# Performance work log

Measured on AMD Instinct MI355X. Metric: run time of the kernel, lower is better.

The kernel has to match this reference:

```python
import jax, jax.numpy as jnp
import numpy as np

ALPHA, BETA = 0.5, 0.25
DELTA_AGG, DELTA_DIS = 0.5, 3.0
OHEM_RATIO = 3
MAX_INST = 8  # instance ids in [0, MAX_INST); 0 = background
NEG_INF = -1e10


def _safe_norm(sq):
    # sqrt with zero-safe gradient; returns 0 where sq == 0
    return jnp.sqrt(jnp.where(sq > 0, sq, 1.0)) * (sq > 0)


def _agg_dis_single(sim, gt_text, gt_kernel):
    # sim: [4, N] float, gt_text/gt_kernel: [N] int32 instance ids
    lab = jnp.arange(1, MAX_INST)                                  # [K]
    kmask = (gt_kernel[None, :] == lab[:, None]).astype(sim.dtype)  # [K, N]
    tmask = gt_text[None, :] == lab[:, None]                        # [K, N] bool
    kcount = kmask.sum(1)
    tcount = tmask.sum(1).astype(sim.dtype)
    valid = (kcount > 0) & (tcount > 0)                             # [K]
    # per-instance kernel centroid G_kernel: masked segment mean of sim vectors
    G = (kmask @ sim.T) / jnp.maximum(kcount, 1.0)[:, None]         # [K, 4]
    # loss_agg: distance of each text pixel's sim vector to its kernel centroid
    diff = sim.T[None, :, :] - G[:, None, :]                        # [K, N, 4]
    d = _safe_norm(jnp.sum(diff * diff, -1))                        # [K, N]
    D = jnp.square(jnp.maximum(d - DELTA_AGG, 0.0))
    per_inst = jnp.sum(jnp.log1p(D) * tmask, 1) / jnp.maximum(tcount, 1.0)
    n_valid = jnp.sum(valid)
    loss_agg = jnp.sum(jnp.where(valid, per_inst, 0.0)) / jnp.maximum(n_valid, 1).astype(sim.dtype)
    # loss_dis: pairwise discrimination between valid kernel centroids
    gd = G[:, None, :] - G[None, :, :]                              # [K, K, 4]
    gnorm = _safe_norm(jnp.sum(gd * gd, -1))
    Dij = jnp.square(jnp.maximum(DELTA_DIS - gnorm, 0.0))
    K = MAX_INST - 1
    idx = jnp.arange(K)
    pair = valid[:, None] & valid[None, :] & (idx[:, None] < idx[None, :])
    s = jnp.sum(jnp.where(pair, jnp.log1p(Dij), 0.0))
    denom = (n_valid * (n_valid - 1)).astype(sim.dtype)  # matches torch: n*(n-1), not #pairs
    loss_dis = jnp.where(n_valid > 1, s / jnp.maximum(denom, 1.0), 0.0)
    return loss_agg, loss_dis


def _ohem_single(score, gt, tm):
    # score/tm: [N] float, gt: [N] int — all flattened
    pos = gt > 0.5
    pos_num = jnp.sum(pos) - jnp.sum(pos & (tm <= 0.5))
    neg = ~pos
    neg_total = jnp.sum(neg)
    neg_num = jnp.minimum(pos_num * OHEM_RATIO, neg_total)
    neg_scores = jnp.where(neg, score, NEG_INF)
    sorted_desc = -jnp.sort(-neg_scores)
    threshold = sorted_desc[jnp.maximum(neg_num - 1, 0)]
    sel = (((score >= threshold) | pos) & (tm > 0.5)).astype(tm.dtype)
    fallback = (pos_num == 0) | (neg_num == 0)
    return jnp.where(fallback, tm, sel)


def _dice(inp, tgt, mask):
    # inp: [B, N] logits, tgt: [B, N] (binarized at 0.5), mask: [B, N]
    p = jax.nn.sigmoid(inp) * mask
    t = (tgt > 0.5).astype(p.dtype) * mask
    a = jnp.sum(p * t, 1)
    b = jnp.sum(p * p, 1) + 1e-3
    c = jnp.sum(t * t, 1) + 1e-3
    return 1.0 - 2.0 * a / (b + c)


def _pan_loss(outputs, labels, training_masks):
    B = outputs.shape[0]
    texts = outputs[:, 0].reshape(B, -1)
    kernels = outputs[:, 1].reshape(B, -1)
    sim = outputs[:, 2:].reshape(B, 4, -1)
    gt_texts = labels[:, 0].reshape(B, -1)
    gt_kernels = labels[:, 1].reshape(B, -1)
    tm = training_masks.reshape(B, -1)

    loss_aggs, loss_diss = jax.vmap(_agg_dis_single)(sim, gt_texts, gt_kernels)

    # OHEM mask is computed on detached scores in the original (numpy round-trip)
    sel_text = jax.vmap(_ohem_single)(jax.lax.stop_gradient(texts), gt_texts, tm)
    loss_texts = _dice(texts, gt_texts, sel_text)

    sel_kernel = jax.lax.stop_gradient(
        ((jax.nn.sigmoid(texts) > 0.5) & (tm > 0.5)).astype(texts.dtype))
    loss_kernels = _dice(kernels, gt_kernels, sel_kernel)

    loss_text = loss_texts.mean()
    loss_kernel = loss_kernels.mean()
    loss_agg = loss_aggs.mean()
    loss_dis = loss_diss.mean()
    loss_all = loss_text + ALPHA * loss_kernel + BETA * (loss_agg + loss_dis)
    return loss_all, loss_text, loss_kernel, loss_agg, loss_dis


def setup_inputs() -> dict:
    key = jax.random.key(0)
    k1, k2, k3 = jax.random.split(key, 3)
    B, H, W = 8, 640, 640
    outputs = jax.random.normal(k1, (B, 6, H, W), dtype=jnp.float32)
    labels = jax.random.randint(k2, (B, 2, H, W), 0, MAX_INST).astype(jnp.int32)
    training_masks = jax.random.uniform(k3, (B, H, W), dtype=jnp.float32)
    return {"outputs": outputs, "labels": labels, "training_masks": training_masks}


def reference(outputs, labels, training_masks):
    return _pan_loss(outputs, labels, training_masks)
```

## Files before the change

kernel.cpp:

```cpp
#include <hip/hip_runtime.h>

#define NPIX 409600
#define NB 8

constexpr int OFF_H0   = 0;
constexpr int OFF_H1   = 2048;
constexpr int OFF_H2   = 4096;
constexpr int OFF_KC   = 5120;
constexpr int OFF_TC   = 5128;
constexpr int OFF_KS   = 5136;
constexpr int OFF_AGG  = 5168;
constexpr int OFF_CPOS = 5176;
constexpr int OFF_CPOSM= 5177;
constexpr int OFF_KN   = 5178;
constexpr int OFF_KNF  = 5179;
constexpr int OFF_FALL = 5180;
constexpr int OFF_NV   = 5181;
constexpr int OFF_VM   = 5182;
constexpr int OFF_LDIS = 5183;
constexpr int OFF_BTN  = 5184;
constexpr int OFF_PFX0 = 5185;
constexpr int OFF_K1   = 5186;
constexpr int OFF_PFX22= 5187;
constexpr int OFF_K2   = 5188;
constexpr int OFF_DICE = 5190;
constexpr int PER_BATCH= 5248;
constexpr int KEYS_BASE= NB * PER_BATCH;
constexpr int HDR_WORDS= NB * PER_BATCH;

__device__ __forceinline__ unsigned mapf(float s) {
  unsigned b = __float_as_uint(s);
  return (b & 0x80000000u) ? ~b : (b | 0x80000000u);
}
__device__ __forceinline__ float unmapf(unsigned u) {
  return __uint_as_float((u & 0x80000000u) ? (u & 0x7FFFFFFFu) : ~u);
}
__device__ __forceinline__ float sigf(float x) {
  return __fdividef(1.f, 1.f + __expf(-x));
}
__device__ __forceinline__ float wredf(float v) {
#pragma unroll
  for (int m = 32; m >= 1; m >>= 1) v += __shfl_xor(v, m, 64);
  return v;
}
__device__ __forceinline__ unsigned wredu(unsigned v) {
#pragma unroll
  for (int m = 32; m >= 1; m >>= 1) v += (unsigned)__shfl_xor((int)v, m, 64);
  return v;
}

__global__ __launch_bounds__(256) void kZ(unsigned* __restrict__ ws) {
  int i = blockIdx.x * 256 + threadIdx.x;
  if (i < HDR_WORDS) ws[i] = 0u;
}

__global__ __launch_bounds__(256) void kXS(const float* __restrict__ out_,
                                           const int* __restrict__ lab_,
                                           const float* __restrict__ tm_,
                                           unsigned* __restrict__ ws) {
  const int b = blockIdx.y;
  unsigned* wsb = ws + (size_t)b * PER_BATCH;
  float* wsbf = (float*)wsb;
  __shared__ __align__(16) unsigned shm[4412];
  const int tid = threadIdx.x, lane = tid & 63, w = tid >> 6;

  if (blockIdx.x < 200) {
    const int bx = blockIdx.x;
    unsigned* sh_h   = shm;
    unsigned* shScan = shm + 2048;
    unsigned* shTC   = shm + 2304;
    float*    shRed  = (float*)(shm + 2336);
    unsigned* shC    = shm + 2372;
    unsigned* shBase = shm + 2380;
    for (int i = tid; i < 2048; i += 256) sh_h[i] = 0u;
    __syncthreads();

    const float4* tx = (const float4*)(out_ + (size_t)b * 6 * NPIX);
    const float4* kr = (const float4*)(out_ + (size_t)b * 6 * NPIX + (size_t)NPIX);
    const int4* gt = (const int4*)(lab_ + (size_t)b * 2 * NPIX);
    const int4* gk = (const int4*)(lab_ + (size_t)b * 2 * NPIX + NPIX);
    const float4* tmv = (const float4*)(tm_ + (size_t)b * NPIX);

    unsigned cpos = 0, cposm = 0, vmask = 0, fmask = 0;
    unsigned tcq[7];
#pragma unroll
    for (int k = 0; k < 7; ++k) tcq[k] = 0u;
    unsigned kreg[8];
    float at = 0.f, btp = 0.f, ct = 0.f, atf = 0.f, btf = 0.f, ctf = 0.f;
    float ak = 0.f, bk = 0.f, ck = 0.f;

#pragma unroll
    for (int it = 0; it < 2; ++it) {
      const int i = it * 51200 + bx * 256 + tid;
      float4 t4 = tx[i]; float4 q4 = kr[i]; int4 g4 = gt[i]; int4 k4 = gk[i]; float4 m4 = tmv[i];
#pragma unroll
      for (int j = 0; j < 4; ++j) {
        float tv = ((const float*)&t4)[j];
        float kv = ((const float*)&q4)[j];
        int gtv = ((const int*)&g4)[j];
        int gkv = ((const int*)&k4)[j];
        float mv = ((const float*)&m4)[j];
        bool pos = gtv > 0;
        bool mh = mv > 0.5f;
        cpos += pos;
        cposm += (pos && !mh);
        unsigned key = mapf(tv);
        kreg[it * 4 + j] = key;
        float sig = sigf(tv);
        if (!pos) {
          vmask |= 1u << (it * 4 + j);
          if (mh) fmask |= 1u << (it * 4 + j);
          atomicAdd(&sh_h[key >> 21], 1u);
        } else if (mh) {
          at += sig; btp += sig * sig; ct += 1.f;
        }
#pragma unroll
        for (int k = 0; k < 7; ++k)
          tcq[k] += (unsigned)__popcll(__ballot(gtv == k + 1));
        float sm = sig * mv;
        btf += sm * sm;
        if (pos) { atf += sm * mv; ctf += mv * mv; }
        if ((tv > 0.f) && mh) {
          float sk = sigf(kv);
          bk += sk * sk;
          if (gkv > 0) { ak += sk; ck += 1.f; }
        }
      }
    }

    unsigned r = wredu(cpos), r2 = wredu(cposm);
    if (lane == 0) { shC[w * 2] = r; shC[w * 2 + 1] = r2; }
    if (lane == 0) {
#pragma unroll
      for (int k = 0; k < 7; ++k) shTC[w * 7 + k] = tcq[k];
    }
    float v9[9] = {at, btp, ct, atf, btf, ctf, ak, bk, ck};
#pragma unroll
    for (int q = 0; q < 9; ++q) {
      float f = wredf(v9[q]);
      if (lane == 0) shRed[w * 9 + q] = f;
    }

    unsigned cnt = (unsigned)__popc(vmask), cntF = (unsigned)__popc(fmask);
    shScan[tid] = cnt | (cntF << 16);
    __syncthreads();
#pragma unroll
    for (int off = 1; off < 256; off <<= 1) {
      unsigned vv = (tid >= off) ? shScan[tid - off] : 0u;
      __syncthreads();
      shScan[tid] += vv;
      __syncthreads();
    }
    if (tid == 0) {
      unsigned tot = shScan[255];
      shBase[0] = atomicAdd(&wsb[OFF_KN], tot & 0xFFFFu);
      shBase[1] = atomicAdd(&wsb[OFF_KNF], tot >> 16);
    }
    for (int i = tid; i < 2048; i += 256) {
      unsigned h = sh_h[i]; if (h) atomicAdd(&wsb[OFF_H0 + i], h);
    }
    if (tid < 7) {
      unsigned s = shTC[tid] + shTC[7 + tid] + shTC[14 + tid] + shTC[21 + tid];
      if (s) atomicAdd(&wsb[OFF_TC + 1 + tid], s);
    } else if (tid >= 16 && tid < 25) {
      int q = tid - 16;
      float s = shRed[q] + shRed[9 + q] + shRed[18 + q] + shRed[27 + q];
      atomicAdd(&wsbf[OFF_DICE + q], s);
    } else if (tid == 30) {
      atomicAdd(&wsb[OFF_CPOS], shC[0] + shC[2] + shC[4] + shC[6]);
    } else if (tid == 31) {
      atomicAdd(&wsb[OFF_CPOSM], shC[1] + shC[3] + shC[5] + shC[7]);
    }
    __syncthreads();
    unsigned gA = shBase[0] + (shScan[tid] & 0xFFFFu) - cnt;
    unsigned gF = shBase[1] + (shScan[tid] >> 16) - cntF;
    unsigned* keys = ws + KEYS_BASE + (size_t)b * NPIX;
#pragma unroll
    for (int s = 0; s < 8; ++s)
      if (vmask & (1u << s)) { keys[gA] = kreg[s]; ++gA; }
#pragma unroll
    for (int s = 0; s < 8; ++s)
      if (fmask & (1u << s)) { keys[NPIX - 1 - gF] = kreg[s]; ++gF; }
  } else {
    const bool lo = blockIdx.x < 328;
    const int bx = lo ? (blockIdx.x - 200) : (blockIdx.x - 328);
    float* L = (float*)shm;
    float* L2 = (float*)(shm + 4112);
    unsigned* sh_kcw = shm + 4384;
    for (int i = tid; i < 4112; i += 256) L[i] = 0.f;
    __syncthreads();

    const float4* sa = (const float4*)(out_ + (size_t)b * 6 * NPIX + (size_t)(lo ? 2 : 4) * NPIX);
    const float4* sb = (const float4*)(out_ + (size_t)b * 6 * NPIX + (size_t)(lo ? 3 : 5) * NPIX);
    const int4* gkk = (const int4*)(lab_ + (size_t)b * 2 * NPIX + NPIX);

    unsigned kcq[7];
#pragma unroll
    for (int k = 0; k < 7; ++k) kcq[k] = 0u;

    const int nv = NPIX / 4;
    for (int i = bx * 256 + tid; i < nv; i += 128 * 256) {
      int4 k4 = gkk[i];
      float4 a0 = sa[i], a1 = sb[i];
#pragma unroll
      for (int j = 0; j < 4; ++j) {
        int gkv = ((const int*)&k4)[j];
        if (lo) {
#pragma unroll
          for (int k = 0; k < 7; ++k)
            kcq[k] += (unsigned)__popcll(__ballot(gkv == k + 1));
        }
        int idx = (gkv > 0) ? (gkv - 1) : 7;
        float2* slot = (float2*)&L[(idx * 257 + tid) * 2];
        float2 rr = *slot;
        rr.x += ((const float*)&a0)[j];
        rr.y += ((const float*)&a1)[j];
        *slot = rr;
      }
    }

    if (lo && lane == 0) {
#pragma unroll
      for (int k = 0; k < 7; ++k) sh_kcw[w * 7 + k] = kcq[k];
    }
    __syncthreads();
    {
      int p = tid & 15, sub = tid >> 4;
      int idx = p & 7, c = (p >> 3) & 1;
      float part = 0.f;
#pragma unroll
      for (int q = 0; q < 16; ++q) part += L[(idx * 257 + (sub + 16 * q)) * 2 + c];
      L2[p * 17 + sub] = part;
    }
    __syncthreads();
    if (tid < 16) {
      float s = 0.f;
#pragma unroll
      for (int q = 0; q < 16; ++q) s += L2[tid * 17 + q];
      int idx = tid & 7, c = (tid >> 3) & 1;
      if (idx < 7 && s != 0.f)
        atomicAdd(&wsbf[OFF_KS + (idx + 1) * 4 + (lo ? 0 : 2) + c], s);
    } else if (lo && tid >= 64 && tid < 71) {
      int k = tid - 64;
      unsigned s = sh_kcw[k] + sh_kcw[7 + k] + sh_kcw[14 + k] + sh_kcw[21 + k];
      if (s) atomicAdd(&wsb[OFF_KC + 1 + k], s);
    }
  }
}

__global__ __launch_bounds__(256) void kGB(const float* __restrict__ out_,
                                           const int* __restrict__ lab_,
                                           unsigned* __restrict__ ws) {
  const int b = blockIdx.y;
  unsigned* wsb = ws + (size_t)b * PER_BATCH;
  float* wsbf = (float*)wsb;
  const int tid = threadIdx.x, lane = tid & 63, w = tid >> 6;

  if (blockIdx.x < 200) {
    __shared__ float sG[32];
    __shared__ float sAgg[4 * 7];
    const int bx = blockIdx.x;
    if (tid < 32) {
      int inst = tid >> 2, c = tid & 3;
      float g = 0.f;
      if (inst >= 1) {
        unsigned kc = wsb[OFF_KC + inst];
        g = wsbf[OFF_KS + inst * 4 + c] / fmaxf((float)kc, 1.f);
      }
      sG[tid] = g;
    }
    __syncthreads();
    const int4* gt = (const int4*)(lab_ + (size_t)b * 2 * NPIX);
    const float4* s0 = (const float4*)(out_ + (size_t)b * 6 * NPIX + 2 * (size_t)NPIX);
    const float4* s1 = (const float4*)(out_ + (size_t)b * 6 * NPIX + 3 * (size_t)NPIX);
    const float4* s2 = (const float4*)(out_ + (size_t)b * 6 * NPIX + 4 * (size_t)NPIX);
    const float4* s3 = (const float4*)(out_ + (size_t)b * 6 * NPIX + 5 * (size_t)NPIX);
    float agg[7];
#pragma unroll
    for (int k = 0; k < 7; ++k) agg[k] = 0.f;
#pragma unroll
    for (int it = 0; it < 2; ++it) {
      const int i = it * 51200 + bx * 256 + tid;
      int4 g4 = gt[i];
      float4 a0 = s0[i], a1 = s1[i], a2 = s2[i], a3 = s3[i];
#pragma unroll
      for (int j = 0; j < 4; ++j) {
        int gtv = ((const int*)&g4)[j];
        bool pos = gtv > 0;
        int kk = pos ? gtv : 0;
        float d0 = ((const float*)&a0)[j] - sG[kk * 4 + 0];
        float d1 = ((const float*)&a1)[j] - sG[kk * 4 + 1];
        float d2 = ((const float*)&a2)[j] - sG[kk * 4 + 2];
        float d3 = ((const float*)&a3)[j] - sG[kk * 4 + 3];
        float sq = d0 * d0 + d1 * d1 + d2 * d2 + d3 * d3;
        float d = (sq > 0.f) ? sqrtf(sq) : 0.f;
        float dd = fmaxf(d - 0.5f, 0.f);
        float lg = pos ? __logf(1.f + dd * dd) : 0.f;
#pragma unroll
        for (int k = 0; k < 7; ++k) agg[k] += (gtv == k + 1) ? lg : 0.f;
      }
    }
#pragma unroll
    for (int k = 0; k < 7; ++k) {
      float f = wredf(agg[k]);
      if (lane == 0) sAgg[w * 7 + k] = f;
    }
    __syncthreads();
    if (tid < 7) {
      float s = sAgg[tid] + sAgg[7 + tid] + sAgg[14 + tid] + sAgg[21 + tid];
      if (s != 0.f) atomicAdd(&wsbf[OFF_AGG + 1 + tid], s);
    }
  } else {
    const int bb = blockIdx.x - 200;
    __shared__ unsigned S[256];
    __shared__ unsigned sh_h1[2048];
    __shared__ unsigned sh_k, sh_pfx0;
    __shared__ int sh_fall;
    if (tid == 0) {
      unsigned cpos = wsb[OFF_CPOS], cposm = wsb[OFF_CPOSM];
      long posnum = (long)cpos - (long)cposm;
      long cneg = (long)NPIX - (long)cpos;
      long negnum = posnum * 3; if (negnum > cneg) negnum = cneg;
      int fall = (posnum == 0) || (negnum == 0);
      wsb[OFF_FALL] = (unsigned)fall;
      sh_fall = fall; sh_k = (unsigned)negnum;
      float G[8][4];
      unsigned nvv = 0, vm = 0;
      for (int k = 1; k < 8; ++k) {
        unsigned kc = wsb[OFF_KC + k], tc = wsb[OFF_TC + k];
        float inv = 1.f / fmaxf((float)kc, 1.f);
        for (int c = 0; c < 4; ++c) G[k][c] = wsbf[OFF_KS + k * 4 + c] * inv;
        if (kc > 0 && tc > 0) { vm |= 1u << k; ++nvv; }
      }
      wsb[OFF_NV] = nvv; wsb[OFF_VM] = vm;
      float s = 0.f;
      for (int i = 1; i < 8; ++i) {
        if (!((vm >> i) & 1)) continue;
        for (int j = i + 1; j < 8; ++j) {
          if (!((vm >> j) & 1)) continue;
          float sq = 0.f;
          for (int c = 0; c < 4; ++c) { float d = G[i][c] - G[j][c]; sq += d * d; }
          float gn = (sq > 0.f) ? sqrtf(sq) : 0.f;
          float dd = fmaxf(3.0f - gn, 0.f);
          s += log1pf(dd * dd);
        }
      }
      float denom = (float)(nvv * (nvv > 0 ? nvv - 1u : 0u));
      wsbf[OFF_LDIS] = (nvv > 1) ? (s / fmaxf(denom, 1.f)) : 0.f;
    }
    __syncthreads();
    if (sh_fall) return;
    unsigned myp = 0;
#pragma unroll
    for (int j = 0; j < 8; ++j) myp += wsb[OFF_H0 + tid * 8 + j];
    S[tid] = myp;
    __syncthreads();
#pragma unroll
    for (int off = 1; off < 256; off <<= 1) {
      unsigned v = (tid + off < 256) ? S[tid + off] : 0u;
      __syncthreads();
      S[tid] += v;
      __syncthreads();
    }
    {
      unsigned k = sh_k;
      unsigned suf = S[tid], sufn = suf - myp;
      if (suf >= k && sufn < k) {
        unsigned kk = k - sufn;
        unsigned cum2 = 0; int bin = tid * 8;
#pragma unroll
        for (int j = 7; j >= 0; --j) {
          unsigned h = wsb[OFF_H0 + tid * 8 + j]; cum2 += h;
          if (cum2 >= kk) { bin = tid * 8 + j; kk -= (cum2 - h); break; }
        }
        sh_pfx0 = (unsigned)bin;
        wsb[OFF_PFX0] = (unsigned)bin;
        wsb[OFF_K1] = kk;
      }
    }
    __syncthreads();
    const unsigned pfx = sh_pfx0;
    const unsigned kn = wsb[OFF_KN];
    for (int i = tid; i < 2048; i += 256) sh_h1[i] = 0u;
    __syncthreads();
    const unsigned* keys = ws + KEYS_BASE + (size_t)b * NPIX;
    for (unsigned i = bb * 256u + tid; i < kn; i += 16u * 256u) {
      unsigned key = keys[i];
      if ((key >> 21) == pfx) atomicAdd(&sh_h1[(key >> 10) & 0x7FFu], 1u);
    }
    __syncthreads();
    for (int i = tid; i < 2048; i += 256) {
      unsigned v = sh_h1[i]; if (v) atomicAdd(&wsb[OFF_H1 + i], v);
    }
  }
}

__global__ __launch_bounds__(256) void kCD(unsigned* __restrict__ ws) {
  const int b = blockIdx.y;
  unsigned* wsb = ws + (size_t)b * PER_BATCH;
  if (wsb[OFF_FALL]) return;
  __shared__ unsigned S[256];
  __shared__ unsigned sh_h2[1024];
  __shared__ unsigned sh_p22;
  const int tid = threadIdx.x;
  unsigned myp = 0;
#pragma unroll
  for (int j = 0; j < 8; ++j) myp += wsb[OFF_H1 + tid * 8 + j];
  S[tid] = myp;
  __syncthreads();
#pragma unroll
  for (int off = 1; off < 256; off <<= 1) {
    unsigned v = (tid + off < 256) ? S[tid + off] : 0u;
    __syncthreads();
    S[tid] += v;
    __syncthreads();
  }
  {
    unsigned k = wsb[OFF_K1];
    unsigned suf = S[tid], sufn = suf - myp;
    if (suf >= k && sufn < k) {
      unsigned kk = k - sufn;
      unsigned cum2 = 0; int bin = tid * 8;
#pragma unroll
      for (int j = 7; j >= 0; --j) {
        unsigned h = wsb[OFF_H1 + tid * 8 + j]; cum2 += h;
        if (cum2 >= kk) { bin = tid * 8 + j; kk -= (cum2 - h); break; }
      }
      unsigned p22 = (wsb[OFF_PFX0] << 11) | (unsigned)bin;
      sh_p22 = p22;
      wsb[OFF_PFX22] = p22;
      wsb[OFF_K2] = kk;
    }
  }
  __syncthreads();
  const unsigned pfx22 = sh_p22;
  const unsigned kn = wsb[OFF_KN];
  for (int i = tid; i < 1024; i += 256) sh_h2[i] = 0u;
  __syncthreads();
  const unsigned* keys = ws + KEYS_BASE + (size_t)b * NPIX;
  for (unsigned i = blockIdx.x * 256u + tid; i < kn; i += 16u * 256u) {
    unsigned key = keys[i];
    if ((key >> 10) == pfx22) atomicAdd(&sh_h2[key & 0x3FFu], 1u);
  }
  __syncthreads();
  for (int i = tid; i < 1024; i += 256) {
    unsigned v = sh_h2[i]; if (v) atomicAdd(&wsb[OFF_H2 + i], v);
  }
}

__global__ __launch_bounds__(256) void kEF(unsigned* __restrict__ ws) {
  const int b = blockIdx.y;
  unsigned* wsb = ws + (size_t)b * PER_BATCH;
  float* wsbf = (float*)wsb;
  if (wsb[OFF_FALL]) return;
  __shared__ unsigned S[256];
  __shared__ unsigned sh_thk;
  __shared__ float sF[4];
  const int tid = threadIdx.x, lane = tid & 63, w = tid >> 6;
  unsigned myp = 0;
#pragma unroll
  for (int j = 0; j < 4; ++j) myp += wsb[OFF_H2 + tid * 4 + j];
  S[tid] = myp;
  __syncthreads();
#pragma unroll
  for (int off = 1; off < 256; off <<= 1) {
    unsigned v = (tid + off < 256) ? S[tid + off] : 0u;
    __syncthreads();
    S[tid] += v;
    __syncthreads();
  }
  {
    unsigned k = wsb[OFF_K2];
    unsigned suf = S[tid], sufn = suf - myp;
    if (suf >= k && sufn < k) {
      unsigned kk = k - sufn;
      unsigned cum2 = 0; int bin = tid * 4;
#pragma unroll
      for (int j = 3; j >= 0; --j) {
        unsigned h = wsb[OFF_H2 + tid * 4 + j]; cum2 += h;
        if (cum2 >= kk) { bin = tid * 4 + j; break; }
      }
      sh_thk = (wsb[OFF_PFX22] << 10) | (unsigned)bin;
    }
  }
  __syncthreads();
  const unsigned thkey = sh_thk;
  const unsigned knF = wsb[OFF_KNF];
  const unsigned* listB = ws + KEYS_BASE + (size_t)b * NPIX + (NPIX - knF);
  float part = 0.f;
  for (unsigned i = blockIdx.x * 256u + tid; i < knF; i += 16u * 256u) {
    unsigned key = listB[i];
    if (key >= thkey) {
      float sg = sigf(unmapf(key));
      part += sg * sg;
    }
  }
  part = wredf(part);
  if (lane == 0) sF[w] = part;
  __syncthreads();
  if (tid == 0) {
    float s = sF[0] + sF[1] + sF[2] + sF[3];
    if (s != 0.f) atomicAdd(&wsbf[OFF_BTN], s);
  }
}

__global__ void kH(const unsigned* __restrict__ ws, float* __restrict__ out) {
  __shared__ float sv[4][8];
  const int b = threadIdx.x;
  if (b < 8) {
    const unsigned* wsb = ws + (size_t)b * PER_BATCH;
    const float* wsbf = (const float*)wsb;
    int fall = (int)wsb[OFF_FALL];
    float at, bt, ct;
    if (fall) {
      at = wsbf[OFF_DICE + 3]; bt = wsbf[OFF_DICE + 4]; ct = wsbf[OFF_DICE + 5];
    } else {
      at = wsbf[OFF_DICE + 0];
      bt = wsbf[OFF_DICE + 1] + wsbf[OFF_BTN];
      ct = wsbf[OFF_DICE + 2];
    }
    float lt = 1.f - 2.f * at / ((bt + 1e-3f) + (ct + 1e-3f));
    float ak = wsbf[OFF_DICE + 6], bk = wsbf[OFF_DICE + 7] + 1e-3f, ck = wsbf[OFF_DICE + 8] + 1e-3f;
    float lk = 1.f - 2.f * ak / (bk + ck);
    unsigned vm = wsb[OFF_VM], nvv = wsb[OFF_NV];
    float s = 0.f;
    for (int k = 1; k < 8; ++k)
      if ((vm >> k) & 1) s += wsbf[OFF_AGG + k] / fmaxf((float)wsb[OFF_TC + k], 1.f);
    float la = s / fmaxf((float)nvv, 1.f);
    float ld = wsbf[OFF_LDIS];
    sv[0][b] = lt; sv[1][b] = lk; sv[2][b] = la; sv[3][b] = ld;
  }
  __syncthreads();
  if (threadIdx.x == 0) {
    float mt = 0.f, mk = 0.f, ma = 0.f, md = 0.f;
    for (int i = 0; i < 8; ++i) { mt += sv[0][i]; mk += sv[1][i]; ma += sv[2][i]; md += sv[3][i]; }
    mt *= 0.125f; mk *= 0.125f; ma *= 0.125f; md *= 0.125f;
    out[0] = mt + 0.5f * mk + 0.25f * (ma + md);
    out[1] = mt;
    out[2] = mk;
    out[3] = ma;
    out[4] = md;
  }
}

extern "C" void kernel_launch(void* const* d_in, const int* in_sizes, int n_in,
                              void* d_out, int out_size, void* d_ws, size_t ws_size,
                              hipStream_t stream) {
  const float* outputs = (const float*)d_in[0];
  const int* labels = (const int*)d_in[1];
  const float* tm = (const float*)d_in[2];
  unsigned* ws = (unsigned*)d_ws;
  float* out = (float*)d_out;

  dim3 blk(256);
  kZ<<<(HDR_WORDS + 255) / 256, blk, 0, stream>>>(ws);
  kXS<<<dim3(456, NB), blk, 0, stream>>>(outputs, labels, tm, ws);
  kGB<<<dim3(216, NB), blk, 0, stream>>>(outputs, labels, ws);
  kCD<<<dim3(16, NB), blk, 0, stream>>>(ws);
  kEF<<<dim3(16, NB), blk, 0, stream>>>(ws);
  kH<<<1, 64, 0, stream>>>(ws, out);
}
```

Baseline: 88.54 us.

## Replace LDS per-thread bins and ballot counts with register accumulators and wave reductions

The kernel-centroid blocks previously scattered each pixel's sim values into a per-thread LDS bin table and then reduced it through two LDS passes. They now keep seven per-instance register accumulators selected by predicate, followed by wave shuffle reductions. Per-pixel ballot/popcount instance counting in both block types is also replaced by per-lane counters reduced once at the end. This shrinks shared memory from about 17KB to under 10KB, which may raise occupancy and removes LDS traffic. The cost is more per-pixel ALU work (7-way predicated FMAs) and extra registers.

```diff
diff --git a/kernel.cpp b/kernel.cpp
--- a/kernel.cpp
+++ b/kernel.cpp
@@ -61,7 +61,7 @@
   const int b = blockIdx.y;
   unsigned* wsb = ws + (size_t)b * PER_BATCH;
   float* wsbf = (float*)wsb;
-  __shared__ __align__(16) unsigned shm[4412];
+  __shared__ __align__(16) unsigned shm[2384];
   const int tid = threadIdx.x, lane = tid & 63, w = tid >> 6;
 
   if (blockIdx.x < 200) {
@@ -69,9 +69,9 @@
     unsigned* sh_h   = shm;
     unsigned* shScan = shm + 2048;
     unsigned* shTC   = shm + 2304;
-    float*    shRed  = (float*)(shm + 2336);
-    unsigned* shC    = shm + 2372;
-    unsigned* shBase = shm + 2380;
+    float*    shRed  = (float*)(shm + 2332);
+    unsigned* shC    = shm + 2368;
+    unsigned* shBase = shm + 2376;
     for (int i = tid; i < 2048; i += 256) sh_h[i] = 0u;
     __syncthreads();
 
@@ -116,7 +116,7 @@
         }
 #pragma unroll
         for (int k = 0; k < 7; ++k)
-          tcq[k] += (unsigned)__popcll(__ballot(gtv == k + 1));
+          tcq[k] += (gtv == k + 1);
         float sm = sig * mv;
         btf += sm * sm;
         if (pos) { atf += sm * mv; ctf += mv * mv; }
@@ -130,9 +130,10 @@
 
     unsigned r = wredu(cpos), r2 = wredu(cposm);
     if (lane == 0) { shC[w * 2] = r; shC[w * 2 + 1] = r2; }
-    if (lane == 0) {
-#pragma unroll
-      for (int k = 0; k < 7; ++k) shTC[w * 7 + k] = tcq[k];
+#pragma unroll
+    for (int k = 0; k < 7; ++k) {
+      unsigned rt = wredu(tcq[k]);
+      if (lane == 0) shTC[w * 7 + k] = rt;
     }
     float v9[9] = {at, btp, ct, atf, btf, ctf, ak, bk, ck};
 #pragma unroll
@@ -184,19 +185,17 @@
   } else {
     const bool lo = blockIdx.x < 328;
     const int bx = lo ? (blockIdx.x - 200) : (blockIdx.x - 328);
-    float* L = (float*)shm;
-    float* L2 = (float*)(shm + 4112);
-    unsigned* sh_kcw = shm + 4384;
-    for (int i = tid; i < 4112; i += 256) L[i] = 0.f;
-    __syncthreads();
+    float* shSred = (float*)shm;
+    unsigned* shScnt = shm + 64;
 
     const float4* sa = (const float4*)(out_ + (size_t)b * 6 * NPIX + (size_t)(lo ? 2 : 4) * NPIX);
     const float4* sb = (const float4*)(out_ + (size_t)b * 6 * NPIX + (size_t)(lo ? 3 : 5) * NPIX);
     const int4* gkk = (const int4*)(lab_ + (size_t)b * 2 * NPIX + NPIX);
 
+    float ka[7], kb2[7];
     unsigned kcq[7];
 #pragma unroll
-    for (int k = 0; k < 7; ++k) kcq[k] = 0u;
+    for (int k = 0; k < 7; ++k) { ka[k] = 0.f; kb2[k] = 0.f; kcq[k] = 0u; }
 
     const int nv = NPIX / 4;
     for (int i = bx * 256 + tid; i < nv; i += 128 * 256) {
@@ -205,44 +204,39 @@
 #pragma unroll
       for (int j = 0; j < 4; ++j) {
         int gkv = ((const int*)&k4)[j];
-        if (lo) {
-#pragma unroll
-          for (int k = 0; k < 7; ++k)
-            kcq[k] += (unsigned)__popcll(__ballot(gkv == k + 1));
+        float va = ((const float*)&a0)[j];
+        float vb = ((const float*)&a1)[j];
+#pragma unroll
+        for (int k = 0; k < 7; ++k) {
+          bool m = (gkv == k + 1);
+          float sel = m ? 1.f : 0.f;
+          ka[k] += sel * va;
+          kb2[k] += sel * vb;
+          kcq[k] += m;
         }
-        int idx = (gkv > 0) ? (gkv - 1) : 7;
-        float2* slot = (float2*)&L[(idx * 257 + tid) * 2];
-        float2 rr = *slot;
-        rr.x += ((const float*)&a0)[j];
-        rr.y += ((const float*)&a1)[j];
-        *slot = rr;
-      }
-    }
-
-    if (lo && lane == 0) {
-#pragma unroll
-      for (int k = 0; k < 7; ++k) sh_kcw[w * 7 + k] = kcq[k];
-    }
-    __syncthreads();
-    {
-      int p = tid & 15, sub = tid >> 4;
-      int idx = p & 7, c = (p >> 3) & 1;
-      float part = 0.f;
-#pragma unroll
-      for (int q = 0; q < 16; ++q) part += L[(idx * 257 + (sub + 16 * q)) * 2 + c];
-      L2[p * 17 + sub] = part;
-    }
-    __syncthreads();
-    if (tid < 16) {
-      float s = 0.f;
-#pragma unroll
-      for (int q = 0; q < 16; ++q) s += L2[tid * 17 + q];
-      int idx = tid & 7, c = (tid >> 3) & 1;
-      if (idx < 7 && s != 0.f)
-        atomicAdd(&wsbf[OFF_KS + (idx + 1) * 4 + (lo ? 0 : 2) + c], s);
-    } else if (lo && tid >= 64 && tid < 71) {
-      int k = tid - 64;
-      unsigned s = sh_kcw[k] + sh_kcw[7 + k] + sh_kcw[14 + k] + sh_kcw[21 + k];
+      }
+    }
+
+#pragma unroll
+    for (int k = 0; k < 7; ++k) {
+      float fa = wredf(ka[k]);
+      float fb = wredf(kb2[k]);
+      if (lane == 0) { shSred[w * 14 + k] = fa; shSred[w * 14 + 7 + k] = fb; }
+      if (lo) {
+        unsigned rc = wredu(kcq[k]);
+        if (lane == 0) shScnt[w * 7 + k] = rc;
+      }
+    }
+    __syncthreads();
+    if (tid < 14) {
+      int k = tid % 7, c = tid / 7;
+      float s = shSred[c * 7 + k] + shSred[14 + c * 7 + k] +
+                shSred[28 + c * 7 + k] + shSred[42 + c * 7 + k];
+      if (s != 0.f)
+        atomicAdd(&wsbf[OFF_KS + (k + 1) * 4 + (lo ? 0 : 2) + c], s);
+    } else if (lo && tid >= 16 && tid < 23) {
+      int k = tid - 16;
+      unsigned s = shScnt[k] + shScnt[7 + k] + shScnt[14 + k] + shScnt[21 + k];
       if (s) atomicAdd(&wsb[OFF_KC + 1 + k], s);
     }
   }
```

New measurement: 91.37 us. 1.03x slower.
